# Kernel optimization log

Measured on AMD Instinct MI355X. Metric: run time of the kernel, lower is better.

The kernel has to match this reference:

```python
import jax, jax.numpy as jnp
import numpy as np

K = 3        # kernel_size
STRIDE = 1
PAD = 1
DIL = 1


def setup_inputs() -> dict:
    key = jax.random.key(0)
    k1, k2, k3 = jax.random.split(key, 3)
    B, C, H, W = 8, 256, 64, 64
    O = 256
    x = jax.random.normal(k1, (B, C, H, W), jnp.float32)
    # offset conv: Conv2d(C, 2*K*K, K, stride, pad) with bias
    w_off = jax.random.normal(k2, (2 * K * K, C, K, K), jnp.float32) * 0.01
    b_off = jnp.zeros((2 * K * K,), jnp.float32)
    # DeformConv weight (mmcv DeformConv has no bias)
    w_dcn = jax.random.normal(k3, (O, C, K, K), jnp.float32) * (1.0 / np.sqrt(C * K * K))
    return {"x": x, "w_off": w_off, "b_off": b_off, "w_dcn": w_dcn}


def _conv(x, w):
    return jax.lax.conv_general_dilated(
        x, w, window_strides=(STRIDE, STRIDE),
        padding=[(PAD, PAD), (PAD, PAD)], rhs_dilation=(DIL, DIL),
        dimension_numbers=("NCHW", "OIHW", "NCHW"))


def _bilinear(img_flat, y, x, H, W):
    # img_flat: [C, H*W]; y, x: [KK, Ho, Wo] float sampling coords
    y0 = jnp.floor(y)
    x0 = jnp.floor(x)
    out = jnp.zeros((img_flat.shape[0],) + y.shape, img_flat.dtype)
    for dy in (0.0, 1.0):
        for dx in (0.0, 1.0):
            yi = y0 + dy
            xi = x0 + dx
            wgt = (1.0 - jnp.abs(y - yi)) * (1.0 - jnp.abs(x - xi))
            valid = (yi >= 0) & (yi < H) & (xi >= 0) & (xi < W)
            yc = jnp.clip(yi, 0, H - 1).astype(jnp.int32)
            xc = jnp.clip(xi, 0, W - 1).astype(jnp.int32)
            idx = yc * W + xc                       # [KK,Ho,Wo]
            g = jnp.take(img_flat, idx.reshape(-1), axis=1)
            g = g.reshape((img_flat.shape[0],) + y.shape)  # [C,KK,Ho,Wo]
            out = out + g * (wgt * valid)[None]
    return out


def reference(x, w_off, b_off, w_dcn):
    B, C, H, W = x.shape
    O = w_dcn.shape[0]
    # 1) predict offsets: [B, 2*K*K, Ho, Wo], channel order (ky,kx) pairs per tap
    offset = _conv(x, w_off) + b_off[None, :, None, None]
    Ho, Wo = offset.shape[2], offset.shape[3]
    off = offset.reshape(B, K * K, 2, Ho, Wo)
    off_y = off[:, :, 0]   # [B,KK,Ho,Wo]
    off_x = off[:, :, 1]
    # 2) base sampling grid for a standard conv
    ky, kx = jnp.meshgrid(jnp.arange(K), jnp.arange(K), indexing="ij")
    ky = ky.reshape(-1).astype(x.dtype)   # [KK]
    kx = kx.reshape(-1).astype(x.dtype)
    hy = (jnp.arange(Ho) * STRIDE - PAD).astype(x.dtype)
    wx = (jnp.arange(Wo) * STRIDE - PAD).astype(x.dtype)
    base_y = hy[None, :, None] + (ky * DIL)[:, None, None]  # [KK,Ho,1]
    base_x = wx[None, None, :] + (kx * DIL)[:, None, None]  # [KK,1,Wo]
    sy = off_y + base_y[None]   # [B,KK,Ho,Wo]
    sx = off_x + base_x[None]
    # 3) bilinear gather: sampled patches [B,C,KK,Ho,Wo]
    img_flat = x.reshape(B, C, H * W)
    sampled = jax.vmap(lambda im, yy, xx: _bilinear(im, yy, xx, H, W))(img_flat, sy, sx)
    # 4) weighted sum over (C, kernel taps)
    out = jnp.einsum("bckhw,ock->bohw", sampled, w_dcn.reshape(O, C, K * K))
    return out
```

## Files before the change

### kernel.cpp

```cpp
#include <hip/hip_runtime.h>
#include <hip/hip_bf16.h>


#define HW 64
#define CCH 256
#define OCH 256
#define BB 8
#define KDIM 2304

typedef __attribute__((ext_vector_type(8))) short bf16x8;
typedef __attribute__((ext_vector_type(8))) unsigned short u16x8;
typedef __attribute__((ext_vector_type(4))) float f32x4;
typedef __attribute__((ext_vector_type(2))) float f32x2;
typedef __attribute__((ext_vector_type(4))) unsigned short u16x4;
typedef __attribute__((ext_vector_type(4))) unsigned int u32x4;

static __device__ inline unsigned short f2bf(float f) {
  unsigned u = __builtin_bit_cast(unsigned, f);
  u += 0x7FFFu + ((u >> 16) & 1u);
  return (unsigned short)(u >> 16);
}
static __device__ inline float bf2f(unsigned short s) {
  return __builtin_bit_cast(float, (unsigned)s << 16);
}
static __device__ inline unsigned cvt_pk_bf16(float lo, float hi) {
  unsigned r;
  asm("v_cvt_pk_bf16_f32 %0, %1, %2" : "=v"(r) : "v"(lo), "v"(hi));
  return r;
}

#define GLL16(gsrc, ldst)                                                      \
  __builtin_amdgcn_global_load_lds(                                           \
      (const __attribute__((address_space(1))) void*)(gsrc),                  \
      (__attribute__((address_space(3))) void*)(ldst), 16, 0, 0)

static __device__ inline int xcd_swz256(int bid) {
  return (bid & 7) * 32 + (bid >> 3);
}

__global__ __launch_bounds__(256) void prep_xpose(
    const float* __restrict__ x, const float* __restrict__ w_dcn,
    const float* __restrict__ w_off, unsigned short* __restrict__ xTbf,
    unsigned short* __restrict__ W2, unsigned short* __restrict__ Wop,
    unsigned short* __restrict__ zp) {
  const int tid = threadIdx.x;
  const int bid = blockIdx.x;
  if (bid < 2048) {
    __shared__ float t[64][65];
    const int ct = bid & 3;
    const int pt = (bid >> 2) & 63;
    const int b = bid >> 8;
#pragma unroll
    for (int i = 0; i < 16; ++i) {
      int cl = i * 4 + (tid >> 6);
      int p = tid & 63;
      t[cl][p] = x[(((b << 8) + ct * 64 + cl) << 12) + pt * 64 + p];
    }
    __syncthreads();
#pragma unroll
    for (int i = 0; i < 4; ++i) {
      int pl = i * 16 + (tid >> 4);
      int c4 = (tid & 15) * 4;
      u16x4 v;
      v[0] = f2bf(t[c4][pl]);
      v[1] = f2bf(t[c4 + 1][pl]);
      v[2] = f2bf(t[c4 + 2][pl]);
      v[3] = f2bf(t[c4 + 3][pl]);
      *(u16x4*)(xTbf + (((size_t)((b << 12) + pt * 64 + pl)) << 8) + ct * 64 +
                c4) = v;
    }
  } else {
    int i = (bid - 2048) * 256 + tid;
    if (i < 9 * 256 * 256) {
      int o = i / KDIM;
      int r = i - o * KDIM;
      int kk = r >> 8, c = r & 255;
      W2[i] = f2bf(w_dcn[((o << 8) + c) * 9 + kk]);
    }
    if (i < 32 * KDIM) {
      int n = i / KDIM;
      int r = i - n * KDIM;
      int kk = r >> 8, c = r & 255;
      Wop[i] = (n < 18) ? f2bf(w_off[((n << 8) + c) * 9 + kk]) : (unsigned short)0;
    }
    if (i < 512) zp[i] = 0;
  }
}

__global__ __launch_bounds__(512) void offset_gemm(
    const unsigned short* __restrict__ xTbf, const unsigned short* __restrict__ Wop,
    const unsigned short* __restrict__ zp, const float* __restrict__ b_off,
    float* __restrict__ off_buf) {
  __shared__ short ldsA[2][128 * 32];
  __shared__ short ldsB[2][32 * 32];
  const int tid = threadIdx.x;
  const int lane = tid & 63;
  const int wid = __builtin_amdgcn_readfirstlane(tid >> 6);
  const int m0 = xcd_swz256(blockIdx.x) * 128;
  const int b = m0 >> 12;
  const unsigned short* xb = xTbf + ((size_t)b << 20);

  const int rS = tid >> 2;
  const int cS = tid & 3;
  const int posS = (m0 & 4095) + rS;
  const int hS = posS >> 6, wS = posS & 63;
  const int scS = (cS ^ ((rS >> 1) & 3)) * 8;
  const int rB = tid >> 2;
  const unsigned short* srcB =
      Wop + (size_t)rB * KDIM + ((tid & 3) ^ ((rB >> 1) & 3)) * 8;

  const int l15 = lane & 15, l4 = lane >> 4;
  const int rA = wid * 16 + l15;
  const int offA = rA * 32 + ((l4 ^ ((rA >> 1) & 3)) << 3);
  int offB[2];
#pragma unroll
  for (int f = 0; f < 2; ++f) {
    const int rb = f * 16 + l15;
    offB[f] = rb * 32 + ((l4 ^ ((rb >> 1) & 3)) << 3);
  }

  const f32x4 z = {0.f, 0.f, 0.f, 0.f};
  f32x4 acc[2];
  acc[0] = z;
  acc[1] = z;

  auto stage = [&](int buf, int t) {
    const int kk = t >> 3;
    const int c0 = (t & 7) * 32;
    const int dy = kk / 3 - 1, dx = kk - (kk / 3) * 3 - 1;
    const int y = hS + dy, xx = wS + dx;
    const bool valid = ((unsigned)y < 64u) && ((unsigned)xx < 64u);
    const unsigned short* src =
        valid ? xb + ((((y << 6) + xx) << 8) + c0 + scS) : zp + scS;
    GLL16(src, &ldsA[buf][tid * 8]);
    if (tid < 128) GLL16(srcB + t * 32, &ldsB[buf][tid * 8]);
  };

  stage(0, 0);
  __syncthreads();

  for (int t = 0; t < 72; ++t) {
    const int buf = t & 1;
    if (t < 71) stage(buf ^ 1, t + 1);
    bf16x8 af, bfr[2];
    af = *(const bf16x8*)&ldsA[buf][offA];
#pragma unroll
    for (int f = 0; f < 2; ++f) bfr[f] = *(const bf16x8*)&ldsB[buf][offB[f]];
#pragma unroll
    for (int j = 0; j < 2; ++j)
      acc[j] = __builtin_amdgcn_mfma_f32_16x16x32_bf16(af, bfr[j], acc[j],
                                                       0, 0, 0);
    __syncthreads();
  }

#pragma unroll
  for (int j = 0; j < 2; ++j) {
    const int col = j * 16 + l15;
    if (col < 18) {
      const float bias = b_off[col];
#pragma unroll
      for (int rr = 0; rr < 4; ++rr) {
        const int m = m0 + wid * 16 + l4 * 4 + rr;
        off_buf[(size_t)m * 18 + col] = acc[j][rr] + bias;
      }
    }
  }
}

__global__ __launch_bounds__(512, 2) void dcn_fused(
    const unsigned short* __restrict__ xTbf, const float* __restrict__ off_buf,
    const unsigned short* __restrict__ W2, float* __restrict__ out) {
  __shared__ f32x2 slyx[128][9];
  __shared__ u16x4 spos[128][9];
  __shared__ short ldsA[2][128 * 64];
  __shared__ short ldsB[2][256 * 64];

  const int tid = threadIdx.x;
  const int lane = tid & 63;
  const int wid = __builtin_amdgcn_readfirstlane(tid >> 6);
  const int m0 = xcd_swz256(blockIdx.x) * 128;
  const int b = m0 >> 12;
  const unsigned short* xb = xTbf + ((size_t)b << 20);

  for (int idx = tid; idx < 128 * 9; idx += 512) {
    const int r = idx / 9, k = idx - (idx / 9) * 9;
    const int ky = k / 3, kx = k - ky * 3;
    const int pos = (m0 & 4095) + r;
    const int h = pos >> 6, w = pos & 63;
    const float offy = off_buf[(size_t)(m0 + r) * 18 + 2 * k];
    const float offx = off_buf[(size_t)(m0 + r) * 18 + 2 * k + 1];
    const float sy = offy + (float)(h - 1 + ky);
    const float sx = offx + (float)(w - 1 + kx);
    const float y0f = floorf(sy), x0f = floorf(sx);
    const int y0 = (int)y0f, x0 = (int)x0f;
    const int y1 = y0 + 1, x1 = x0 + 1;
    const unsigned vy0 = ((unsigned)y0 < 64u), vy1 = ((unsigned)y1 < 64u);
    const unsigned vx0 = ((unsigned)x0 < 64u), vx1 = ((unsigned)x1 < 64u);
    const int y0c = min(max(y0, 0), HW - 1), y1c = min(max(y1, 0), HW - 1);
    const int x0c = min(max(x0, 0), HW - 1), x1c = min(max(x1, 0), HW - 1);
    f32x2 lyx;
    lyx[0] = sy - y0f;
    lyx[1] = sx - x0f;
    u16x4 pp;
    pp[0] = (unsigned short)(((y0c << 6) + x0c) | ((vy0 & vx0) << 15));
    pp[1] = (unsigned short)(((y0c << 6) + x1c) | ((vy0 & vx1) << 15));
    pp[2] = (unsigned short)(((y1c << 6) + x0c) | ((vy1 & vx0) << 15));
    pp[3] = (unsigned short)(((y1c << 6) + x1c) | ((vy1 & vx1) << 15));
    slyx[r][k] = lyx;
    spos[r][k] = pp;
  }

  const int r = tid >> 2, q = tid & 3;
  const int dstA0 = r * 64 + (((2 * q) ^ (r & 7)) << 3);
  const int dstA1 = r * 64 + (((2 * q + 1) ^ (r & 7)) << 3);

  const unsigned short* srcBp[4];
  int dstB[4];
#pragma unroll
  for (int g = 0; g < 4; ++g) {
    const int idx = g * 512 + tid;
    const int row = idx >> 3, c = idx & 7;
    srcBp[g] = W2 + (size_t)row * KDIM + ((c ^ (row & 7)) << 3);
    dstB[g] = idx * 8;
  }

  const int l15 = lane & 15, l4 = lane >> 4;
  const int wm = wid & 1, wn = wid >> 1;
  int offA[4][2], offB[4][2];
#pragma unroll
  for (int f = 0; f < 4; ++f) {
    const int rA = wm * 64 + f * 16 + l15;
    const int rB = wn * 64 + f * 16 + l15;
#pragma unroll
    for (int h = 0; h < 2; ++h) {
      offA[f][h] = rA * 64 + (((h * 4 + l4) ^ (rA & 7)) << 3);
      offB[f][h] = rB * 64 + (((h * 4 + l4) ^ (rB & 7)) << 3);
    }
  }

  const f32x4 z = {0.f, 0.f, 0.f, 0.f};
  f32x4 acc[4][4];
#pragma unroll
  for (int i = 0; i < 4; ++i)
#pragma unroll
    for (int j = 0; j < 4; ++j) acc[i][j] = z;

  __syncthreads();

  f32x4 wv;
  int av[4];
  auto load_params = [&](int tap) {
    const f32x2 lyx = slyx[r][tap];
    const u16x4 pp = spos[r][tap];
    const float ly = lyx[0], lx = lyx[1];
#pragma unroll
    for (int e = 0; e < 4; ++e) av[e] = (int)(pp[e] & 0x0FFFu) << 8;
    wv[0] = (1.f - ly) * (1.f - lx) * (float)(pp[0] >> 15);
    wv[1] = (1.f - ly) * lx * (float)(pp[1] >> 15);
    wv[2] = ly * (1.f - lx) * (float)(pp[2] >> 15);
    wv[3] = ly * lx * (float)(pp[3] >> 15);
  };

  u16x8 gc0[2], gc1[2], gc2[2], gc3[2];
  f32x4 gw;

  auto issue_gathers = [&](int t) {
    const int cb = ((t & 3) << 6) + q * 16;
#pragma unroll
    for (int h = 0; h < 2; ++h) {
      gc0[h] = *(const u16x8*)(xb + av[0] + cb + h * 8);
      gc1[h] = *(const u16x8*)(xb + av[1] + cb + h * 8);
      gc2[h] = *(const u16x8*)(xb + av[2] + cb + h * 8);
      gc3[h] = *(const u16x8*)(xb + av[3] + cb + h * 8);
    }
    gw = wv;
  };

  auto lerp_store = [&](int buf) {
    short* base = ldsA[buf];
#pragma unroll
    for (int h = 0; h < 2; ++h) {
      u32x4 wds;
#pragma unroll
      for (int e = 0; e < 4; ++e) {
        const float f0 = gw[0] * bf2f(gc0[h][2 * e]) + gw[1] * bf2f(gc1[h][2 * e]) +
                         gw[2] * bf2f(gc2[h][2 * e]) + gw[3] * bf2f(gc3[h][2 * e]);
        const float f1 = gw[0] * bf2f(gc0[h][2 * e + 1]) +
                         gw[1] * bf2f(gc1[h][2 * e + 1]) +
                         gw[2] * bf2f(gc2[h][2 * e + 1]) +
                         gw[3] * bf2f(gc3[h][2 * e + 1]);
        wds[e] = cvt_pk_bf16(f0, f1);
      }
      *(u32x4*)&base[h == 0 ? dstA0 : dstA1] = wds;
    }
  };

  load_params(0);
  issue_gathers(0);
  lerp_store(0);
#pragma unroll
  for (int g = 0; g < 4; ++g) GLL16(srcBp[g], &ldsB[0][dstB[g]]);
  __syncthreads();

  for (int t = 0; t < 36; ++t) {
    const int buf = t & 1;
    if (t < 35) {
      const int tn = t + 1;
#pragma unroll
      for (int g = 0; g < 4; ++g) GLL16(srcBp[g] + tn * 64, &ldsB[buf ^ 1][dstB[g]]);
      if ((tn & 3) == 0) load_params(tn >> 2);
      issue_gathers(tn);
    }
#pragma unroll
    for (int h = 0; h < 2; ++h) {
      bf16x8 af[4], bfr[4];
#pragma unroll
      for (int f = 0; f < 4; ++f) {
        af[f] = *(const bf16x8*)&ldsA[buf][offA[f][h]];
        bfr[f] = *(const bf16x8*)&ldsB[buf][offB[f][h]];
      }
#pragma unroll
      for (int i = 0; i < 4; ++i)
#pragma unroll
        for (int j = 0; j < 4; ++j)
          acc[i][j] = __builtin_amdgcn_mfma_f32_16x16x32_bf16(af[i], bfr[j],
                                                              acc[i][j], 0, 0, 0);
    }
    if (t < 35) lerp_store(buf ^ 1);
    __syncthreads();
  }

#pragma unroll
  for (int i = 0; i < 4; ++i) {
    const int m = m0 + wm * 64 + i * 16 + l4 * 4;
    const int bb = m >> 12;
    const int pos = m & 4095;
#pragma unroll
    for (int j = 0; j < 4; ++j) {
      const int o = wn * 64 + j * 16 + l15;
      *(f32x4*)(out + (((size_t)bb * OCH + o) << 12) + pos) = acc[i][j];
    }
  }
}

extern "C" void kernel_launch(void* const* d_in, const int* in_sizes, int n_in,
                              void* d_out, int out_size, void* d_ws,
                              size_t ws_size, hipStream_t stream) {
  const float* x = (const float*)d_in[0];
  const float* w_off = (const float*)d_in[1];
  const float* b_off = (const float*)d_in[2];
  const float* w_dcn = (const float*)d_in[3];
  float* out = (float*)d_out;

  char* ws = (char*)d_ws;
  float* off_buf = (float*)(ws);
  unsigned short* Wop = (unsigned short*)(ws + 2359296);
  unsigned short* zp = (unsigned short*)(ws + 2506752);
  unsigned short* W2 = (unsigned short*)(ws + 2507776);
  unsigned short* xTbf = (unsigned short*)(ws + 3687424);

  prep_xpose<<<4352, 256, 0, stream>>>(x, w_dcn, w_off, xTbf, W2, Wop, zp);
  offset_gemm<<<256, 512, 0, stream>>>(xTbf, Wop, zp, b_off, off_buf);
  dcn_fused<<<256, 512, 0, stream>>>(xTbf, off_buf, W2, out);
}
```

Before: 119.8 us.

## Gather A fragments directly into registers and give each wave full output width

```diff
diff --git a/kernel.cpp b/kernel.cpp
--- a/kernel.cpp
+++ b/kernel.cpp
@@ -172,8 +172,7 @@
     const unsigned short* __restrict__ W2, float* __restrict__ out) {
   __shared__ f32x2 slyx[128][9];
   __shared__ u16x4 spos[128][9];
-  __shared__ short ldsA[2][128 * 64];
-  __shared__ short ldsB[2][256 * 64];
+  __shared__ short ldsB[2][256 * 32];
 
   const int tid = threadIdx.x;
   const int lane = tid & 63;
@@ -210,48 +209,38 @@
     spos[r][k] = pp;
   }
 
-  const int r = tid >> 2, q = tid & 3;
-  const int dstA0 = r * 64 + (((2 * q) ^ (r & 7)) << 3);
-  const int dstA1 = r * 64 + (((2 * q + 1) ^ (r & 7)) << 3);
-
-  const unsigned short* srcBp[4];
-  int dstB[4];
-#pragma unroll
-  for (int g = 0; g < 4; ++g) {
+  const int l15 = lane & 15, l4 = lane >> 4;
+  const int l48 = l4 * 8;
+  const int rlane = wid * 16 + l15;
+
+  const unsigned short* srcBp[2];
+#pragma unroll
+  for (int g = 0; g < 2; ++g) {
     const int idx = g * 512 + tid;
-    const int row = idx >> 3, c = idx & 7;
-    srcBp[g] = W2 + (size_t)row * KDIM + ((c ^ (row & 7)) << 3);
-    dstB[g] = idx * 8;
-  }
-
-  const int l15 = lane & 15, l4 = lane >> 4;
-  const int wm = wid & 1, wn = wid >> 1;
-  int offA[4][2], offB[4][2];
-#pragma unroll
-  for (int f = 0; f < 4; ++f) {
-    const int rA = wm * 64 + f * 16 + l15;
-    const int rB = wn * 64 + f * 16 + l15;
-#pragma unroll
-    for (int h = 0; h < 2; ++h) {
-      offA[f][h] = rA * 64 + (((h * 4 + l4) ^ (rA & 7)) << 3);
-      offB[f][h] = rB * 64 + (((h * 4 + l4) ^ (rB & 7)) << 3);
-    }
+    const int row = idx >> 2, c = idx & 3;
+    srcBp[g] = W2 + (size_t)row * KDIM + ((c ^ ((row >> 1) & 3)) << 3);
+  }
+  const int dstB0 = tid * 8, dstB1 = (512 + tid) * 8;
+
+  int offB[16];
+#pragma unroll
+  for (int j = 0; j < 16; ++j) {
+    const int rB = j * 16 + l15;
+    offB[j] = rB * 32 + ((l4 ^ ((rB >> 1) & 3)) << 3);
   }
 
   const f32x4 z = {0.f, 0.f, 0.f, 0.f};
-  f32x4 acc[4][4];
-#pragma unroll
-  for (int i = 0; i < 4; ++i)
-#pragma unroll
-    for (int j = 0; j < 4; ++j) acc[i][j] = z;
+  f32x4 acc[16];
+#pragma unroll
+  for (int j = 0; j < 16; ++j) acc[j] = z;
 
   __syncthreads();
 
   f32x4 wv;
   int av[4];
   auto load_params = [&](int tap) {
-    const f32x2 lyx = slyx[r][tap];
-    const u16x4 pp = spos[r][tap];
+    const f32x2 lyx = slyx[rlane][tap];
+    const u16x4 pp = spos[rlane][tap];
     const float ly = lyx[0], lx = lyx[1];
 #pragma unroll
     for (int e = 0; e < 4; ++e) av[e] = (int)(pp[e] & 0x0FFFu) << 8;
@@ -261,84 +250,90 @@
     wv[3] = ly * lx * (float)(pp[3] >> 15);
   };
 
-  u16x8 gc0[2], gc1[2], gc2[2], gc3[2];
-  f32x4 gw;
-
-  auto issue_gathers = [&](int t) {
-    const int cb = ((t & 3) << 6) + q * 16;
-#pragma unroll
-    for (int h = 0; h < 2; ++h) {
-      gc0[h] = *(const u16x8*)(xb + av[0] + cb + h * 8);
-      gc1[h] = *(const u16x8*)(xb + av[1] + cb + h * 8);
-      gc2[h] = *(const u16x8*)(xb + av[2] + cb + h * 8);
-      gc3[h] = *(const u16x8*)(xb + av[3] + cb + h * 8);
-    }
-    gw = wv;
+  auto lerp_frag = [&](const u16x8& c0, const u16x8& c1, const u16x8& c2,
+                       const u16x8& c3, const f32x4& w) -> bf16x8 {
+    u32x4 words;
+#pragma unroll
+    for (int e = 0; e < 4; ++e) {
+      const float f0 = w[0] * bf2f(c0[2 * e]) + w[1] * bf2f(c1[2 * e]) +
+                       w[2] * bf2f(c2[2 * e]) + w[3] * bf2f(c3[2 * e]);
+      const float f1 = w[0] * bf2f(c0[2 * e + 1]) + w[1] * bf2f(c1[2 * e + 1]) +
+                       w[2] * bf2f(c2[2 * e + 1]) + w[3] * bf2f(c3[2 * e + 1]);
+      words[e] = cvt_pk_bf16(f0, f1);
+    }
+    return __builtin_bit_cast(bf16x8, words);
   };
 
-  auto lerp_store = [&](int buf) {
-    short* base = ldsA[buf];
-#pragma unroll
-    for (int h = 0; h < 2; ++h) {
-      u32x4 wds;
-#pragma unroll
-      for (int e = 0; e < 4; ++e) {
-        const float f0 = gw[0] * bf2f(gc0[h][2 * e]) + gw[1] * bf2f(gc1[h][2 * e]) +
-                         gw[2] * bf2f(gc2[h][2 * e]) + gw[3] * bf2f(gc3[h][2 * e]);
-        const float f1 = gw[0] * bf2f(gc0[h][2 * e + 1]) +
-                         gw[1] * bf2f(gc1[h][2 * e + 1]) +
-                         gw[2] * bf2f(gc2[h][2 * e + 1]) +
-                         gw[3] * bf2f(gc3[h][2 * e + 1]);
-        wds[e] = cvt_pk_bf16(f0, f1);
-      }
-      *(u32x4*)&base[h == 0 ? dstA0 : dstA1] = wds;
-    }
-  };
+  u16x8 gA[4], gB[4];
+  f32x4 wA, wB;
 
   load_params(0);
-  issue_gathers(0);
-  lerp_store(0);
-#pragma unroll
-  for (int g = 0; g < 4; ++g) GLL16(srcBp[g], &ldsB[0][dstB[g]]);
-  __syncthreads();
-
-  for (int t = 0; t < 36; ++t) {
-    const int buf = t & 1;
-    if (t < 35) {
-      const int tn = t + 1;
-#pragma unroll
-      for (int g = 0; g < 4; ++g) GLL16(srcBp[g] + tn * 64, &ldsB[buf ^ 1][dstB[g]]);
-      if ((tn & 3) == 0) load_params(tn >> 2);
-      issue_gathers(tn);
-    }
-#pragma unroll
-    for (int h = 0; h < 2; ++h) {
-      bf16x8 af[4], bfr[4];
-#pragma unroll
-      for (int f = 0; f < 4; ++f) {
-        af[f] = *(const bf16x8*)&ldsA[buf][offA[f][h]];
-        bfr[f] = *(const bf16x8*)&ldsB[buf][offB[f][h]];
-      }
-#pragma unroll
-      for (int i = 0; i < 4; ++i)
-#pragma unroll
-        for (int j = 0; j < 4; ++j)
-          acc[i][j] = __builtin_amdgcn_mfma_f32_16x16x32_bf16(af[i], bfr[j],
-                                                              acc[i][j], 0, 0, 0);
-    }
-    if (t < 35) lerp_store(buf ^ 1);
-    __syncthreads();
-  }
-
-#pragma unroll
-  for (int i = 0; i < 4; ++i) {
-    const int m = m0 + wm * 64 + i * 16 + l4 * 4;
+  gA[0] = *(const u16x8*)(xb + av[0] + l48);
+  gA[1] = *(const u16x8*)(xb + av[1] + l48);
+  gA[2] = *(const u16x8*)(xb + av[2] + l48);
+  gA[3] = *(const u16x8*)(xb + av[3] + l48);
+  wA = wv;
+  GLL16(srcBp[0], &ldsB[0][dstB0]);
+  GLL16(srcBp[1], &ldsB[0][dstB1]);
+  asm volatile("s_waitcnt vmcnt(0) lgkmcnt(0)" ::: "memory");
+  __builtin_amdgcn_s_barrier();
+  __builtin_amdgcn_sched_barrier(0);
+
+#define FSTEP(T, CIN, WIN, COUT, WOUT)                                         \
+  {                                                                            \
+    GLL16(srcBp[0] + ((T) + 1) * 32, &ldsB[((T) + 1) & 1][dstB0]);             \
+    GLL16(srcBp[1] + ((T) + 1) * 32, &ldsB[((T) + 1) & 1][dstB1]);             \
+    __builtin_amdgcn_sched_barrier(0);                                         \
+    if ((((T) + 1) & 7) == 0) load_params(((T) + 1) >> 3);                     \
+    {                                                                          \
+      const int chb = ((((T) + 1) & 7) << 5) + l48;                            \
+      COUT[0] = *(const u16x8*)(xb + av[0] + chb);                             \
+      COUT[1] = *(const u16x8*)(xb + av[1] + chb);                             \
+      COUT[2] = *(const u16x8*)(xb + av[2] + chb);                             \
+      COUT[3] = *(const u16x8*)(xb + av[3] + chb);                             \
+      WOUT = wv;                                                               \
+    }                                                                          \
+    const bf16x8 afrag = lerp_frag(CIN[0], CIN[1], CIN[2], CIN[3], WIN);       \
+    bf16x8 bfr[16];                                                            \
+    _Pragma("unroll") for (int j = 0; j < 16; ++j)                             \
+        bfr[j] = *(const bf16x8*)&ldsB[(T) & 1][offB[j]];                      \
+    __builtin_amdgcn_s_setprio(1);                                             \
+    _Pragma("unroll") for (int j = 0; j < 16; ++j)                             \
+        acc[j] = __builtin_amdgcn_mfma_f32_16x16x32_bf16(afrag, bfr[j],        \
+                                                         acc[j], 0, 0, 0);     \
+    __builtin_amdgcn_s_setprio(0);                                             \
+    asm volatile("s_waitcnt vmcnt(4) lgkmcnt(0)" ::: "memory");                \
+    __builtin_amdgcn_s_barrier();                                              \
+    __builtin_amdgcn_sched_barrier(0);                                         \
+  }
+
+  int t = 0;
+  for (int it = 0; it < 35; ++it) {
+    FSTEP(t, gA, wA, gB, wB) ++t;
+    FSTEP(t, gB, wB, gA, wA) ++t;
+  }
+  FSTEP(70, gA, wA, gB, wB)
+#undef FSTEP
+
+  {
+    const bf16x8 afrag = lerp_frag(gB[0], gB[1], gB[2], gB[3], wB);
+    bf16x8 bfr[16];
+#pragma unroll
+    for (int j = 0; j < 16; ++j) bfr[j] = *(const bf16x8*)&ldsB[1][offB[j]];
+#pragma unroll
+    for (int j = 0; j < 16; ++j)
+      acc[j] = __builtin_amdgcn_mfma_f32_16x16x32_bf16(afrag, bfr[j], acc[j],
+                                                       0, 0, 0);
+  }
+
+  {
+    const int m = m0 + wid * 16 + l4 * 4;
     const int bb = m >> 12;
     const int pos = m & 4095;
 #pragma unroll
-    for (int j = 0; j < 4; ++j) {
-      const int o = wn * 64 + j * 16 + l15;
-      *(f32x4*)(out + (((size_t)bb * OCH + o) << 12) + pos) = acc[i][j];
+    for (int j = 0; j < 16; ++j) {
+      const int o = j * 16 + l15;
+      *(f32x4*)(out + (((size_t)bb * OCH + o) << 12) + pos) = acc[j];
     }
   }
 }
```

Result: slower. 145.1 us (+21.1%).
